# Performance work log

Measured on AMD Instinct MI355X. Metric: run time of the kernel, lower is better.

Reference implementation:

```python
import jax, jax.numpy as jnp
import numpy as np

N, IN_DIM, OUT_DIM, HEADS = 8192, 256, 256, 2
C = OUT_DIM // HEADS  # per-head channel dim (concat=True)
ALPHA = 0.2
NEG = -9e15


def setup_inputs() -> dict:
    key = jax.random.key(0)
    ks = jax.random.split(key, 9)
    h = jax.random.normal(ks[0], (N, IN_DIM), dtype=jnp.float32)
    adj = jax.random.randint(ks[1], (N, N), 0, 2, dtype=jnp.int32)
    # torch nn.Linear weights are [out, in]; xavier-like scale
    def xav(k, shape):
        fan_in, fan_out = shape[1], shape[0]
        s = 1.414 * np.sqrt(6.0 / (fan_in + fan_out))
        return jax.random.uniform(k, shape, jnp.float32, -s, s)
    W1 = xav(ks[2], (HEADS * C, IN_DIM))
    W2 = xav(ks[3], (HEADS * C, IN_DIM))
    W3 = xav(ks[4], (HEADS * C, IN_DIM))
    b1 = jnp.zeros((HEADS * C,), jnp.float32)
    b2 = jnp.zeros((HEADS * C,), jnp.float32)
    b3 = jnp.zeros((HEADS * C,), jnp.float32)
    sa = 1.414 * np.sqrt(6.0 / (HEADS + 2 * C))
    a = jax.random.uniform(ks[5], (HEADS, 2 * C), jnp.float32, -sa, sa)
    return {"h": h, "adj": adj, "W1": W1, "b1": b1, "W2": W2, "b2": b2,
            "W3": W3, "b3": b3, "a": a}


def reference(h, adj, W1, b1, W2, b2, W3, b3, a):
    n = h.shape[0]
    W1h = (h @ W1.T + b1).reshape(n, HEADS, C)  # [N,H,C]
    W2h = (h @ W2.T + b2).reshape(n, HEADS, C)
    W3h = (h @ W3.T + b3).reshape(n, HEADS, C)
    # eij = a . [W1h_i || W2h_j] decomposes into per-node scores
    a1, a2 = a[:, :C], a[:, C:]
    s1 = jnp.einsum('nhc,hc->nh', W1h, a1)  # [N,H]
    s2 = jnp.einsum('nhc,hc->nh', W2h, a2)  # [N,H]
    e = jax.nn.leaky_relu(s1[:, None, :] + s2[None, :, :], ALPHA)  # [N,N,H]
    e = jnp.where(adj[:, :, None] == 1, e, NEG)
    att = jax.nn.softmax(e, axis=1)  # softmax over source dim j (dim=1)
    # dropout is identity in eval mode (training=False)
    h_prime = jnp.einsum('ijh,jhc->ihc', att, W3h)  # [N,H,C]
    return h_prime.reshape(n, HEADS * C)
```

## Files before the change

kernel.cpp:

```cpp
#include <hip/hip_runtime.h>
#include <hip/hip_bf16.h>

#define NN 8192
#define LOG2E 1.44269504088896f
#define S_SPLIT 8
#define JC 1024
#define NT 32

typedef __attribute__((ext_vector_type(8))) short short8;
typedef __attribute__((ext_vector_type(4))) float f32x4;

static __device__ __forceinline__ float bf2f(unsigned short u) {
    union { unsigned int i; float f; } v; v.i = ((unsigned int)u) << 16; return v.f;
}
static __device__ __forceinline__ unsigned short f2bf(float f) {
    union { float f; unsigned int i; } v; v.f = f;
    unsigned int lsb = (v.i >> 16) & 1u;
    v.i += 0x7fffu + lsb;
    return (unsigned short)(v.i >> 16);
}
static __device__ __forceinline__ unsigned int cvtpk(float lo, float hi) {
    unsigned int r;
    asm("v_cvt_pk_bf16_f32 %0, %1, %2" : "=v"(r) : "v"(lo), "v"(hi));
    return r;
}
static __device__ __forceinline__ float fexp2(float x) { return __builtin_amdgcn_exp2f(x); }

static __device__ __forceinline__ void cvt8(const float* __restrict__ p, short8& hi, short8& lo) {
    float4 u = *(const float4*)p;
    float4 v = *(const float4*)(p + 4);
    float f[8] = {u.x, u.y, u.z, u.w, v.x, v.y, v.z, v.w};
#pragma unroll
    for (int j = 0; j < 8; ++j) {
        unsigned short hb = f2bf(f[j]);
        hi[j] = (short)hb;
        lo[j] = (short)f2bf(f[j] - bf2f(hb));
    }
}

__global__ __launch_bounds__(256) void pack_kernel(const int* __restrict__ adj,
                                                   unsigned int* __restrict__ abits,
                                                   const float* __restrict__ W3,
                                                   unsigned short* __restrict__ w3hi,
                                                   unsigned short* __restrict__ w3lo) {
    int b = blockIdx.x;
    if (b < 8192) {
        int w = b * 256 + threadIdx.x;
        const int* src = adj + (size_t)w * 32;
        unsigned int bits = 0;
#pragma unroll
        for (int k = 0; k < 8; ++k) {
            int4 v = *(const int4*)(src + k * 4);
            bits |= (unsigned int)(v.x & 1) << (k * 4 + 0);
            bits |= (unsigned int)(v.y & 1) << (k * 4 + 1);
            bits |= (unsigned int)(v.z & 1) << (k * 4 + 2);
            bits |= (unsigned int)(v.w & 1) << (k * 4 + 3);
        }
        abits[w] = bits;
    } else {
        int i = (b - 8192) * 256 + threadIdx.x;
        float f = W3[i];
        unsigned short hb = f2bf(f);
        w3hi[i] = hb;
        w3lo[i] = f2bf(f - bf2f(hb));
    }
}

__global__ void prep_partial(const float* __restrict__ W1, const float* __restrict__ W2,
                             const float* __restrict__ a,
                             float* __restrict__ v1p, float* __restrict__ v2p) {
    int b = blockIdx.x;
    int t = threadIdx.x;
    int hh = t >> 8, k = t & 255;
    int c0 = (b & 7) * 16;
    const float* W = (b < 8) ? W1 : W2;
    int aoff = (b < 8) ? 0 : 128;
    float acc = 0.f;
    for (int c = c0; c < c0 + 16; ++c)
        acc += W[(size_t)(hh * 128 + c) * 256 + k] * a[hh * 256 + aoff + c];
    ((b < 8) ? v1p : v2p)[(b & 7) * 512 + t] = acc;
}

__global__ void prep_reduce(const float* __restrict__ b1, const float* __restrict__ b2,
                            const float* __restrict__ a,
                            const float* __restrict__ v1p, const float* __restrict__ v2p,
                            float* __restrict__ v1, float* __restrict__ v2, float* __restrict__ bd) {
    int t = threadIdx.x;
    float a1 = 0.f, a2 = 0.f;
    for (int b = 0; b < 8; ++b) { a1 += v1p[b * 512 + t]; a2 += v2p[b * 512 + t]; }
    v1[t] = a1;
    v2[t] = a2;
    int g = t >> 7;
    int hh = g >> 1, which = g & 1, c = t & 127;
    float prod = which ? b2[hh * 128 + c] * a[hh * 256 + 128 + c]
                       : b1[hh * 128 + c] * a[hh * 256 + c];
#pragma unroll
    for (int off = 1; off < 64; off <<= 1) prod += __shfl_xor(prod, off);
    __shared__ float ws[8];
    if ((t & 63) == 0) ws[t >> 6] = prod;
    __syncthreads();
    if (t < 4) bd[t] = ws[2 * t] + ws[2 * t + 1];
}

__global__ __launch_bounds__(256) void s_kernel(const float* __restrict__ hmat,
                         const float* __restrict__ v1, const float* __restrict__ v2,
                         const float* __restrict__ bd,
                         float* __restrict__ s1o, float* __restrict__ s2o) {
    int w = threadIdx.x >> 6, l = threadIdx.x & 63;
    int n = blockIdx.x * 4 + w;
    float4 hv  = *(const float4*)(hmat + (size_t)n * 256 + l * 4);
    float4 va0 = *(const float4*)(v1 + l * 4);
    float4 va1 = *(const float4*)(v1 + 256 + l * 4);
    float4 vb0 = *(const float4*)(v2 + l * 4);
    float4 vb1 = *(const float4*)(v2 + 256 + l * 4);
    float s10 = hv.x*va0.x + hv.y*va0.y + hv.z*va0.z + hv.w*va0.w;
    float s11 = hv.x*va1.x + hv.y*va1.y + hv.z*va1.z + hv.w*va1.w;
    float s20 = hv.x*vb0.x + hv.y*vb0.y + hv.z*vb0.z + hv.w*vb0.w;
    float s21 = hv.x*vb1.x + hv.y*vb1.y + hv.z*vb1.z + hv.w*vb1.w;
#pragma unroll
    for (int off = 1; off < 64; off <<= 1) {
        s10 += __shfl_xor(s10, off);
        s11 += __shfl_xor(s11, off);
        s20 += __shfl_xor(s20, off);
        s21 += __shfl_xor(s21, off);
    }
    if (l == 0) {
        s1o[n*2 + 0] = (s10 + bd[0]) * LOG2E;
        s1o[n*2 + 1] = (s11 + bd[2]) * LOG2E;
        s2o[n]       = (s20 + bd[1]) * LOG2E;
        s2o[NN + n]  = (s21 + bd[3]) * LOG2E;
    }
}

__global__ __launch_bounds__(256) void w3_kernel(const float* __restrict__ hmat,
                                                 const unsigned short* __restrict__ w3hi,
                                                 const unsigned short* __restrict__ w3lo,
                                                 const float* __restrict__ b3,
                                                 unsigned short* __restrict__ w3b) {
    int tid = threadIdx.x;
    int w = tid >> 6, l = tid & 63;
    int m = l & 15, kq = l >> 4;
    int n0 = (blockIdx.x * 2 + (w & 1)) * 16;
    int c0 = (w >> 1) * 8;
    f32x4 acc[8];
#pragma unroll
    for (int ct = 0; ct < 8; ++ct) acc[ct] = (f32x4){0.f, 0.f, 0.f, 0.f};
    for (int k0 = 0; k0 < 256; k0 += 32) {
        short8 ahi, alo;
        cvt8(hmat + (size_t)(n0 + m) * 256 + k0 + kq * 8, ahi, alo);
#pragma unroll
        for (int ct = 0; ct < 8; ++ct) {
            int c = (c0 + ct) * 16 + m;
            short8 bhi = *(const short8*)&w3hi[(size_t)c * 256 + k0 + kq * 8];
            short8 blo = *(const short8*)&w3lo[(size_t)c * 256 + k0 + kq * 8];
            acc[ct] = __builtin_amdgcn_mfma_f32_16x16x32_bf16(ahi, bhi, acc[ct], 0, 0, 0);
            acc[ct] = __builtin_amdgcn_mfma_f32_16x16x32_bf16(alo, bhi, acc[ct], 0, 0, 0);
            acc[ct] = __builtin_amdgcn_mfma_f32_16x16x32_bf16(ahi, blo, acc[ct], 0, 0, 0);
        }
    }
#pragma unroll
    for (int ct = 0; ct < 8; ++ct) {
        int c = (c0 + ct) * 16 + m;
        float bias = b3[c];
#pragma unroll
        for (int e = 0; e < 4; ++e) {
            int n = n0 + kq * 4 + e;
            size_t idx = ((size_t)(n >> 5) * 16 + (c >> 4)) * 512 + (size_t)((((n >> 3) & 3) * 16 + m) * 8 + (n & 7));
            w3b[idx] = f2bf(acc[ct][e] + bias);
        }
    }
}

__global__ __launch_bounds__(256, 4) void attn_fused(
        const unsigned int* __restrict__ abits, const float* __restrict__ s1a,
        const float* __restrict__ s2h, const unsigned short* __restrict__ w3b,
        unsigned short* __restrict__ pacc, float* __restrict__ pden)
{
    __shared__ float s2t[2][JC];
    __shared__ unsigned int abt[64][33];

    const int tid = threadIdx.x;
    const int ln = tid & 63;
    const int m = ln & 15, kq = ln >> 4;
    const int cg = tid >> 6;
    const int hw = cg >> 1;
    const int sidx = blockIdx.x & 7;
    const int i0 = (blockIdx.x >> 3) * 64;
    const int j0 = sidx * JC;

    float s1r[4];
#pragma unroll
    for (int rt = 0; rt < 4; ++rt) s1r[rt] = s1a[(i0 + rt * 16 + m) * 2 + hw];

    const unsigned short* w3p = w3b + ((size_t)(j0 >> 5) * 16 + cg * 4) * 512 + ln * 8;

    f32x4 acc[4][4];
#pragma unroll
    for (int rt = 0; rt < 4; ++rt)
#pragma unroll
        for (int f = 0; f < 4; ++f) acc[rt][f] = (f32x4){0.f, 0.f, 0.f, 0.f};
    float den[4] = {0.f, 0.f, 0.f, 0.f};

    for (int x = tid; x < 2 * JC; x += 256) {
        int h = x >> 10, j = x & (JC - 1);
        s2t[h][j] = s2h[(size_t)h * NN + j0 + j];
    }
    for (int x = tid; x < 64 * 32; x += 256) {
        int rr = x >> 5, tt = x & 31;
        abt[rr][tt] = abits[(size_t)(i0 + rr) * 256 + (j0 >> 5) + tt];
    }
    __syncthreads();

    for (int t = 0; t < NT; ++t) {
        const unsigned short* bp = w3p + (size_t)t * 8192;
        short8 bf0 = *(const short8*)(bp);
        short8 bf1 = *(const short8*)(bp + 512);
        short8 bf2 = *(const short8*)(bp + 1024);
        short8 bf3 = *(const short8*)(bp + 1536);
        float4 sA = *(const float4*)&s2t[hw][t * 32 + kq * 8];
        float4 sB = *(const float4*)&s2t[hw][t * 32 + kq * 8 + 4];
        float sj[8] = {sA.x, sA.y, sA.z, sA.w, sB.x, sB.y, sB.z, sB.w};
#pragma unroll
        for (int rt = 0; rt < 4; ++rt) {
            unsigned int bits = abt[rt * 16 + m][t] >> (kq * 8);
            const float sr = s1r[rt];
            union { short8 v; unsigned int u[4]; } A;
            float dd = 0.f;
#pragma unroll
            for (int e = 0; e < 4; ++e) {
                float x0 = sr + sj[2 * e];     x0 = fmaxf(x0, 0.2f * x0);
                float x1 = sr + sj[2 * e + 1]; x1 = fmaxf(x1, 0.2f * x1);
                float p0 = (bits >> (2 * e))     & 1u ? fexp2(x0) : 0.f;
                float p1 = (bits >> (2 * e + 1)) & 1u ? fexp2(x1) : 0.f;
                A.u[e] = cvtpk(p0, p1);
                dd += p0 + p1;
            }
            den[rt] += dd;
            __builtin_amdgcn_s_setprio(1);
            acc[rt][0] = __builtin_amdgcn_mfma_f32_16x16x32_bf16(A.v, bf0, acc[rt][0], 0, 0, 0);
            acc[rt][1] = __builtin_amdgcn_mfma_f32_16x16x32_bf16(A.v, bf1, acc[rt][1], 0, 0, 0);
            acc[rt][2] = __builtin_amdgcn_mfma_f32_16x16x32_bf16(A.v, bf2, acc[rt][2], 0, 0, 0);
            acc[rt][3] = __builtin_amdgcn_mfma_f32_16x16x32_bf16(A.v, bf3, acc[rt][3], 0, 0, 0);
            __builtin_amdgcn_s_setprio(0);
        }
    }

#pragma unroll
    for (int rt = 0; rt < 4; ++rt) {
        den[rt] += __shfl_xor(den[rt], 16);
        den[rt] += __shfl_xor(den[rt], 32);
    }
    if ((cg & 1) == 0 && kq == 0) {
#pragma unroll
        for (int rt = 0; rt < 4; ++rt)
            pden[((size_t)sidx * NN + i0 + rt * 16 + m) * 2 + hw] = den[rt];
    }
    size_t pb_ = (size_t)sidx * NN * 256;
#pragma unroll
    for (int rt = 0; rt < 4; ++rt)
#pragma unroll
        for (int e = 0; e < 4; ++e) {
            int row = i0 + rt * 16 + kq * 4 + e;
#pragma unroll
            for (int f = 0; f < 4; ++f) {
                int col = cg * 64 + f * 16 + m;
                __builtin_nontemporal_store(f2bf(acc[rt][f][e]), &pacc[pb_ + (size_t)row * 256 + col]);
            }
        }
}

__global__ void combine_kernel(const unsigned short* __restrict__ pacc, const float* __restrict__ pden,
                               float* __restrict__ out) {
    size_t idx = ((size_t)blockIdx.x * 256 + threadIdx.x) * 8;
    int i = (int)(idx >> 8);
    int c = (int)(idx & 255);
    int hh = c >> 7;
    float acc[8];
#pragma unroll
    for (int e = 0; e < 8; ++e) acc[e] = 0.f;
    float den = 0.f;
    for (int s = 0; s < S_SPLIT; ++s) {
        uint4 v = *(const uint4*)&pacc[(size_t)s * NN * 256 + idx];
        unsigned int uu[4] = {v.x, v.y, v.z, v.w};
#pragma unroll
        for (int q = 0; q < 4; ++q) {
            acc[2*q]   += bf2f((unsigned short)(uu[q] & 0xffff));
            acc[2*q+1] += bf2f((unsigned short)(uu[q] >> 16));
        }
        den += pden[((size_t)s * NN + i) * 2 + hh];
    }
    float r = 1.f / den;
    float4 o0 = {acc[0]*r, acc[1]*r, acc[2]*r, acc[3]*r};
    float4 o1 = {acc[4]*r, acc[5]*r, acc[6]*r, acc[7]*r};
    *(float4*)&out[idx] = o0;
    *(float4*)&out[idx + 4] = o1;
}

extern "C" void kernel_launch(void* const* d_in, const int* in_sizes, int n_in,
                              void* d_out, int out_size, void* d_ws, size_t ws_size,
                              hipStream_t stream) {
    const float* hmat = (const float*)d_in[0];
    const int*   adj  = (const int*)d_in[1];
    const float* W1   = (const float*)d_in[2];
    const float* b1   = (const float*)d_in[3];
    const float* W2   = (const float*)d_in[4];
    const float* b2   = (const float*)d_in[5];
    const float* W3   = (const float*)d_in[6];
    const float* b3   = (const float*)d_in[7];
    const float* a    = (const float*)d_in[8];
    float* out = (float*)d_out;

    char* p = (char*)d_ws;
    float* v1   = (float*)p; p += 2048;
    float* v2   = (float*)p; p += 2048;
    float* bd   = (float*)p; p += 256;
    float* s1   = (float*)p; p += (size_t)NN * 2 * sizeof(float);
    float* s2h  = (float*)p; p += (size_t)NN * 2 * sizeof(float);
    float* v1p  = (float*)p; p += 8 * 512 * sizeof(float);
    float* v2p  = (float*)p; p += 8 * 512 * sizeof(float);
    unsigned short* w3hi = (unsigned short*)p; p += 65536 * 2;
    unsigned short* w3lo = (unsigned short*)p; p += 65536 * 2;
    unsigned short* w3b  = (unsigned short*)p; p += (size_t)NN * 256 * 2;
    unsigned int* abits  = (unsigned int*)p;   p += (size_t)NN * 256 * sizeof(unsigned int);
    float* pden = (float*)p; p += (size_t)S_SPLIT * NN * 2 * sizeof(float);
    unsigned short* pacc = (unsigned short*)p;

    pack_kernel<<<8192 + 256, 256, 0, stream>>>(adj, abits, W3, w3hi, w3lo);
    prep_partial<<<16, 512, 0, stream>>>(W1, W2, a, v1p, v2p);
    prep_reduce<<<1, 512, 0, stream>>>(b1, b2, a, v1p, v2p, v1, v2, bd);
    s_kernel<<<NN / 4, 256, 0, stream>>>(hmat, v1, v2, bd, s1, s2h);
    w3_kernel<<<256, 256, 0, stream>>>(hmat, w3hi, w3lo, b3, w3b);
    attn_fused<<<(NN / 64) * S_SPLIT, 256, 0, stream>>>(abits, s1, s2h, w3b, pacc, pden);
    combine_kernel<<<(NN * 256) / (256 * 8), 256, 0, stream>>>(pacc, pden, out);
}
```

Before: 188.5 us.

## Swap MFMA operand roles so each wave owns 16 rows and all channels

The attention kernel is restructured so each wave handles 16 query rows across all 256 channels. The exp/leaky-relu work for each (row, j) pair is now computed once per wave instead of being split across waves, with W3 as the A operand and probabilities as B. This leaves the output transposed, so partial results are stored channel-major and the combine kernel is rewritten to read that transposed layout and divide by per-row denominators held in shared memory. The intent is to cut redundant VALU exp and bit-extraction work, at the cost of 16 global W3 fragment loads per iteration, higher accumulator register pressure, and scattered 2-byte transposed stores.

```diff
diff --git a/kernel.cpp b/kernel.cpp
--- a/kernel.cpp
+++ b/kernel.cpp
@@ -174,7 +174,7 @@
 __global__ __launch_bounds__(256, 4) void attn_fused(
         const unsigned int* __restrict__ abits, const float* __restrict__ s1a,
         const float* __restrict__ s2h, const unsigned short* __restrict__ w3b,
-        unsigned short* __restrict__ pacc, float* __restrict__ pden)
+        unsigned short* __restrict__ paccT, float* __restrict__ pden)
 {
     __shared__ float s2t[2][JC];
     __shared__ unsigned int abt[64][33];
@@ -182,24 +182,20 @@
     const int tid = threadIdx.x;
     const int ln = tid & 63;
     const int m = ln & 15, kq = ln >> 4;
-    const int cg = tid >> 6;
-    const int hw = cg >> 1;
+    const int wv = tid >> 6;
     const int sidx = blockIdx.x & 7;
     const int i0 = (blockIdx.x >> 3) * 64;
     const int j0 = sidx * JC;
-
-    float s1r[4];
-#pragma unroll
-    for (int rt = 0; rt < 4; ++rt) s1r[rt] = s1a[(i0 + rt * 16 + m) * 2 + hw];
-
-    const unsigned short* w3p = w3b + ((size_t)(j0 >> 5) * 16 + cg * 4) * 512 + ln * 8;
-
-    f32x4 acc[4][4];
-#pragma unroll
-    for (int rt = 0; rt < 4; ++rt)
-#pragma unroll
-        for (int f = 0; f < 4; ++f) acc[rt][f] = (f32x4){0.f, 0.f, 0.f, 0.f};
-    float den[4] = {0.f, 0.f, 0.f, 0.f};
+    const int irow = i0 + wv * 16 + m;
+
+    const float s1r0 = s1a[irow * 2 + 0];
+    const float s1r1 = s1a[irow * 2 + 1];
+    const unsigned short* w3p = w3b + (size_t)(j0 >> 5) * 16 * 512 + ln * 8;
+
+    f32x4 acc[16];
+#pragma unroll
+    for (int ct = 0; ct < 16; ++ct) acc[ct] = (f32x4){0.f, 0.f, 0.f, 0.f};
+    float d0 = 0.f, d1 = 0.f;
 
     for (int x = tid; x < 2 * JC; x += 256) {
         int h = x >> 10, j = x & (JC - 1);
@@ -212,88 +208,87 @@
     __syncthreads();
 
     for (int t = 0; t < NT; ++t) {
+        unsigned int bits = abt[wv * 16 + m][t] >> (kq * 8);
+        float4 sv00 = *(const float4*)&s2t[0][t * 32 + kq * 8];
+        float4 sv01 = *(const float4*)&s2t[0][t * 32 + kq * 8 + 4];
+        float4 sv10 = *(const float4*)&s2t[1][t * 32 + kq * 8];
+        float4 sv11 = *(const float4*)&s2t[1][t * 32 + kq * 8 + 4];
+        float f0[8] = {sv00.x, sv00.y, sv00.z, sv00.w, sv01.x, sv01.y, sv01.z, sv01.w};
+        float f1[8] = {sv10.x, sv10.y, sv10.z, sv10.w, sv11.x, sv11.y, sv11.z, sv11.w};
+        union { short8 v; unsigned int u[4]; } PA, PB;
+        float dd0 = 0.f, dd1 = 0.f;
+#pragma unroll
+        for (int q = 0; q < 4; ++q) {
+            float x0 = s1r0 + f0[2*q];     x0 = fmaxf(x0, 0.2f * x0);
+            float x1 = s1r0 + f0[2*q+1];   x1 = fmaxf(x1, 0.2f * x1);
+            float p0 = (bits >> (2*q))     & 1u ? fexp2(x0) : 0.f;
+            float p1 = (bits >> (2*q+1))   & 1u ? fexp2(x1) : 0.f;
+            PA.u[q] = cvtpk(p0, p1); dd0 += p0 + p1;
+            x0 = s1r1 + f1[2*q];     x0 = fmaxf(x0, 0.2f * x0);
+            x1 = s1r1 + f1[2*q+1];   x1 = fmaxf(x1, 0.2f * x1);
+            p0 = (bits >> (2*q))     & 1u ? fexp2(x0) : 0.f;
+            p1 = (bits >> (2*q+1))   & 1u ? fexp2(x1) : 0.f;
+            PB.u[q] = cvtpk(p0, p1); dd1 += p0 + p1;
+        }
+        d0 += dd0; d1 += dd1;
         const unsigned short* bp = w3p + (size_t)t * 8192;
-        short8 bf0 = *(const short8*)(bp);
-        short8 bf1 = *(const short8*)(bp + 512);
-        short8 bf2 = *(const short8*)(bp + 1024);
-        short8 bf3 = *(const short8*)(bp + 1536);
-        float4 sA = *(const float4*)&s2t[hw][t * 32 + kq * 8];
-        float4 sB = *(const float4*)&s2t[hw][t * 32 + kq * 8 + 4];
-        float sj[8] = {sA.x, sA.y, sA.z, sA.w, sB.x, sB.y, sB.z, sB.w};
-#pragma unroll
-        for (int rt = 0; rt < 4; ++rt) {
-            unsigned int bits = abt[rt * 16 + m][t] >> (kq * 8);
-            const float sr = s1r[rt];
-            union { short8 v; unsigned int u[4]; } A;
-            float dd = 0.f;
-#pragma unroll
-            for (int e = 0; e < 4; ++e) {
-                float x0 = sr + sj[2 * e];     x0 = fmaxf(x0, 0.2f * x0);
-                float x1 = sr + sj[2 * e + 1]; x1 = fmaxf(x1, 0.2f * x1);
-                float p0 = (bits >> (2 * e))     & 1u ? fexp2(x0) : 0.f;
-                float p1 = (bits >> (2 * e + 1)) & 1u ? fexp2(x1) : 0.f;
-                A.u[e] = cvtpk(p0, p1);
-                dd += p0 + p1;
+#pragma unroll
+        for (int ct = 0; ct < 16; ++ct) {
+            short8 aw = *(const short8*)(bp + ct * 512);
+            acc[ct] = __builtin_amdgcn_mfma_f32_16x16x32_bf16(aw, ct < 8 ? PA.v : PB.v, acc[ct], 0, 0, 0);
+        }
+    }
+
+    d0 += __shfl_xor(d0, 16); d0 += __shfl_xor(d0, 32);
+    d1 += __shfl_xor(d1, 16); d1 += __shfl_xor(d1, 32);
+    if (kq == 0) {
+        size_t base = ((size_t)sidx * NN + irow) * 2;
+        pden[base + 0] = d0;
+        pden[base + 1] = d1;
+    }
+    size_t pb_ = (size_t)sidx * NN * 256;
+#pragma unroll
+    for (int ct = 0; ct < 16; ++ct)
+#pragma unroll
+        for (int e = 0; e < 4; ++e) {
+            int c = ct * 16 + kq * 4 + e;
+            __builtin_nontemporal_store(f2bf(acc[ct][e]), &paccT[pb_ + (size_t)c * NN + irow]);
+        }
+}
+
+__global__ __launch_bounds__(256) void combine_kernel(const unsigned short* __restrict__ paccT,
+                                                      const float* __restrict__ pden,
+                                                      float* __restrict__ out) {
+    __shared__ float dsum[32][2];
+    int i0 = blockIdx.x * 32;
+    int c = threadIdx.x;
+    if (threadIdx.x < 64) {
+        int i = threadIdx.x >> 1, h = threadIdx.x & 1;
+        float d = 0.f;
+        for (int s = 0; s < S_SPLIT; ++s) d += pden[((size_t)s * NN + i0 + i) * 2 + h];
+        dsum[i][h] = d;
+    }
+    __syncthreads();
+    float acc[32];
+#pragma unroll
+    for (int e = 0; e < 32; ++e) acc[e] = 0.f;
+    for (int s = 0; s < S_SPLIT; ++s) {
+        const unsigned short* src = paccT + (size_t)s * NN * 256 + (size_t)c * NN + i0;
+#pragma unroll
+        for (int q = 0; q < 4; ++q) {
+            uint4 v = *(const uint4*)(src + q * 8);
+            unsigned int uu[4] = {v.x, v.y, v.z, v.w};
+#pragma unroll
+            for (int w = 0; w < 4; ++w) {
+                acc[q*8 + 2*w]     += bf2f((unsigned short)(uu[w] & 0xffff));
+                acc[q*8 + 2*w + 1] += bf2f((unsigned short)(uu[w] >> 16));
             }
-            den[rt] += dd;
-            __builtin_amdgcn_s_setprio(1);
-            acc[rt][0] = __builtin_amdgcn_mfma_f32_16x16x32_bf16(A.v, bf0, acc[rt][0], 0, 0, 0);
-            acc[rt][1] = __builtin_amdgcn_mfma_f32_16x16x32_bf16(A.v, bf1, acc[rt][1], 0, 0, 0);
-            acc[rt][2] = __builtin_amdgcn_mfma_f32_16x16x32_bf16(A.v, bf2, acc[rt][2], 0, 0, 0);
-            acc[rt][3] = __builtin_amdgcn_mfma_f32_16x16x32_bf16(A.v, bf3, acc[rt][3], 0, 0, 0);
-            __builtin_amdgcn_s_setprio(0);
-        }
-    }
-
-#pragma unroll
-    for (int rt = 0; rt < 4; ++rt) {
-        den[rt] += __shfl_xor(den[rt], 16);
-        den[rt] += __shfl_xor(den[rt], 32);
-    }
-    if ((cg & 1) == 0 && kq == 0) {
-#pragma unroll
-        for (int rt = 0; rt < 4; ++rt)
-            pden[((size_t)sidx * NN + i0 + rt * 16 + m) * 2 + hw] = den[rt];
-    }
-    size_t pb_ = (size_t)sidx * NN * 256;
-#pragma unroll
-    for (int rt = 0; rt < 4; ++rt)
-#pragma unroll
-        for (int e = 0; e < 4; ++e) {
-            int row = i0 + rt * 16 + kq * 4 + e;
-#pragma unroll
-            for (int f = 0; f < 4; ++f) {
-                int col = cg * 64 + f * 16 + m;
-                __builtin_nontemporal_store(f2bf(acc[rt][f][e]), &pacc[pb_ + (size_t)row * 256 + col]);
-            }
-        }
-}
-
-__global__ void combine_kernel(const unsigned short* __restrict__ pacc, const float* __restrict__ pden,
-                               float* __restrict__ out) {
-    size_t idx = ((size_t)blockIdx.x * 256 + threadIdx.x) * 8;
-    int i = (int)(idx >> 8);
-    int c = (int)(idx & 255);
+        }
+    }
     int hh = c >> 7;
-    float acc[8];
-#pragma unroll
-    for (int e = 0; e < 8; ++e) acc[e] = 0.f;
-    float den = 0.f;
-    for (int s = 0; s < S_SPLIT; ++s) {
-        uint4 v = *(const uint4*)&pacc[(size_t)s * NN * 256 + idx];
-        unsigned int uu[4] = {v.x, v.y, v.z, v.w};
-#pragma unroll
-        for (int q = 0; q < 4; ++q) {
-            acc[2*q]   += bf2f((unsigned short)(uu[q] & 0xffff));
-            acc[2*q+1] += bf2f((unsigned short)(uu[q] >> 16));
-        }
-        den += pden[((size_t)s * NN + i) * 2 + hh];
-    }
-    float r = 1.f / den;
-    float4 o0 = {acc[0]*r, acc[1]*r, acc[2]*r, acc[3]*r};
-    float4 o1 = {acc[4]*r, acc[5]*r, acc[6]*r, acc[7]*r};
-    *(float4*)&out[idx] = o0;
-    *(float4*)&out[idx + 4] = o1;
+#pragma unroll
+    for (int i = 0; i < 32; ++i)
+        out[(size_t)(i0 + i) * 256 + c] = acc[i] / dsum[i][hh];
 }
 
 extern "C" void kernel_launch(void* const* d_in, const int* in_sizes, int n_in,
@@ -323,13 +318,13 @@
     unsigned short* w3b  = (unsigned short*)p; p += (size_t)NN * 256 * 2;
     unsigned int* abits  = (unsigned int*)p;   p += (size_t)NN * 256 * sizeof(unsigned int);
     float* pden = (float*)p; p += (size_t)S_SPLIT * NN * 2 * sizeof(float);
-    unsigned short* pacc = (unsigned short*)p;
+    unsigned short* paccT = (unsigned short*)p;
 
     pack_kernel<<<8192 + 256, 256, 0, stream>>>(adj, abits, W3, w3hi, w3lo);
     prep_partial<<<16, 512, 0, stream>>>(W1, W2, a, v1p, v2p);
     prep_reduce<<<1, 512, 0, stream>>>(b1, b2, a, v1p, v2p, v1, v2, bd);
     s_kernel<<<NN / 4, 256, 0, stream>>>(hmat, v1, v2, bd, s1, s2h);
     w3_kernel<<<256, 256, 0, stream>>>(hmat, w3hi, w3lo, b3, w3b);
-    attn_fused<<<(NN / 64) * S_SPLIT, 256, 0, stream>>>(abits, s1, s2h, w3b, pacc, pden);
-    combine_kernel<<<(NN * 256) / (256 * 8), 256, 0, stream>>>(pacc, pden, out);
-}
+    attn_fused<<<(NN / 64) * S_SPLIT, 256, 0, stream>>>(abits, s1, s2h, w3b, paccT, pden);
+    combine_kernel<<<NN / 32, 256, 0, stream>>>(paccT, pden, out);
+}
```

Result: slower. 193.8 us (+2.8%).

## Remap attention waves to row-halves per head to remove duplicated exp work

Applied to the files above, without the earlier changes.

Each wave now owns 32 rows and a full head's 128 output channels, instead of 64 rows and a 64-channel quarter. Each attention probability is therefore computed once per block rather than twice. The cost is twice as many W3 fragment loads per wave per step. The launch grid also becomes 2D, with the j-split on the y axis, which changes block scheduling order.

```diff
diff --git a/kernel.cpp b/kernel.cpp
--- a/kernel.cpp
+++ b/kernel.cpp
@@ -182,24 +182,23 @@
     const int tid = threadIdx.x;
     const int ln = tid & 63;
     const int m = ln & 15, kq = ln >> 4;
-    const int cg = tid >> 6;
-    const int hw = cg >> 1;
-    const int sidx = blockIdx.x & 7;
-    const int i0 = (blockIdx.x >> 3) * 64;
+    const int wv = tid >> 6;
+    const int rg = wv & 1, hd = wv >> 1;
+    const int i0 = blockIdx.x * 64;
+    const int sidx = blockIdx.y;
     const int j0 = sidx * JC;
-
-    float s1r[4];
-#pragma unroll
-    for (int rt = 0; rt < 4; ++rt) s1r[rt] = s1a[(i0 + rt * 16 + m) * 2 + hw];
-
-    const unsigned short* w3p = w3b + ((size_t)(j0 >> 5) * 16 + cg * 4) * 512 + ln * 8;
-
-    f32x4 acc[4][4];
-#pragma unroll
-    for (int rt = 0; rt < 4; ++rt)
-#pragma unroll
-        for (int f = 0; f < 4; ++f) acc[rt][f] = (f32x4){0.f, 0.f, 0.f, 0.f};
-    float den[4] = {0.f, 0.f, 0.f, 0.f};
+    const int rowA = rg * 32 + m, rowB = rg * 32 + 16 + m;
+
+    const float s1r0 = s1a[(i0 + rowA) * 2 + hd];
+    const float s1r1 = s1a[(i0 + rowB) * 2 + hd];
+    const unsigned short* w3p = w3b + ((size_t)(j0 >> 5) * 16 + hd * 8) * 512 + ln * 8;
+
+    f32x4 acc[2][8];
+#pragma unroll
+    for (int rt = 0; rt < 2; ++rt)
+#pragma unroll
+        for (int f = 0; f < 8; ++f) acc[rt][f] = (f32x4){0.f, 0.f, 0.f, 0.f};
+    float dd0 = 0.f, dd1 = 0.f;
 
     for (int x = tid; x < 2 * JC; x += 256) {
         int h = x >> 10, j = x & (JC - 1);
@@ -212,58 +211,49 @@
     __syncthreads();
 
     for (int t = 0; t < NT; ++t) {
+        unsigned int bits0 = abt[rowA][t] >> (kq * 8);
+        unsigned int bits1 = abt[rowB][t] >> (kq * 8);
+        float4 svA = *(const float4*)&s2t[hd][t * 32 + kq * 8];
+        float4 svB = *(const float4*)&s2t[hd][t * 32 + kq * 8 + 4];
+        float sj[8] = {svA.x, svA.y, svA.z, svA.w, svB.x, svB.y, svB.z, svB.w};
+        union { short8 v; unsigned int u[4]; } PA, PB;
+#pragma unroll
+        for (int q = 0; q < 4; ++q) {
+            float x0 = s1r0 + sj[2*q];     x0 = fmaxf(x0, 0.2f * x0);
+            float x1 = s1r0 + sj[2*q+1];   x1 = fmaxf(x1, 0.2f * x1);
+            float p0 = (bits0 >> (2*q))   & 1u ? fexp2(x0) : 0.f;
+            float p1 = (bits0 >> (2*q+1)) & 1u ? fexp2(x1) : 0.f;
+            PA.u[q] = cvtpk(p0, p1); dd0 += p0 + p1;
+            x0 = s1r1 + sj[2*q];     x0 = fmaxf(x0, 0.2f * x0);
+            x1 = s1r1 + sj[2*q+1];   x1 = fmaxf(x1, 0.2f * x1);
+            p0 = (bits1 >> (2*q))   & 1u ? fexp2(x0) : 0.f;
+            p1 = (bits1 >> (2*q+1)) & 1u ? fexp2(x1) : 0.f;
+            PB.u[q] = cvtpk(p0, p1); dd1 += p0 + p1;
+        }
         const unsigned short* bp = w3p + (size_t)t * 8192;
-        short8 bf0 = *(const short8*)(bp);
-        short8 bf1 = *(const short8*)(bp + 512);
-        short8 bf2 = *(const short8*)(bp + 1024);
-        short8 bf3 = *(const short8*)(bp + 1536);
-        float4 sA = *(const float4*)&s2t[hw][t * 32 + kq * 8];
-        float4 sB = *(const float4*)&s2t[hw][t * 32 + kq * 8 + 4];
-        float sj[8] = {sA.x, sA.y, sA.z, sA.w, sB.x, sB.y, sB.z, sB.w};
-#pragma unroll
-        for (int rt = 0; rt < 4; ++rt) {
-            unsigned int bits = abt[rt * 16 + m][t] >> (kq * 8);
-            const float sr = s1r[rt];
-            union { short8 v; unsigned int u[4]; } A;
-            float dd = 0.f;
-#pragma unroll
-            for (int e = 0; e < 4; ++e) {
-                float x0 = sr + sj[2 * e];     x0 = fmaxf(x0, 0.2f * x0);
-                float x1 = sr + sj[2 * e + 1]; x1 = fmaxf(x1, 0.2f * x1);
-                float p0 = (bits >> (2 * e))     & 1u ? fexp2(x0) : 0.f;
-                float p1 = (bits >> (2 * e + 1)) & 1u ? fexp2(x1) : 0.f;
-                A.u[e] = cvtpk(p0, p1);
-                dd += p0 + p1;
-            }
-            den[rt] += dd;
-            __builtin_amdgcn_s_setprio(1);
-            acc[rt][0] = __builtin_amdgcn_mfma_f32_16x16x32_bf16(A.v, bf0, acc[rt][0], 0, 0, 0);
-            acc[rt][1] = __builtin_amdgcn_mfma_f32_16x16x32_bf16(A.v, bf1, acc[rt][1], 0, 0, 0);
-            acc[rt][2] = __builtin_amdgcn_mfma_f32_16x16x32_bf16(A.v, bf2, acc[rt][2], 0, 0, 0);
-            acc[rt][3] = __builtin_amdgcn_mfma_f32_16x16x32_bf16(A.v, bf3, acc[rt][3], 0, 0, 0);
-            __builtin_amdgcn_s_setprio(0);
-        }
-    }
-
-#pragma unroll
-    for (int rt = 0; rt < 4; ++rt) {
-        den[rt] += __shfl_xor(den[rt], 16);
-        den[rt] += __shfl_xor(den[rt], 32);
-    }
-    if ((cg & 1) == 0 && kq == 0) {
-#pragma unroll
-        for (int rt = 0; rt < 4; ++rt)
-            pden[((size_t)sidx * NN + i0 + rt * 16 + m) * 2 + hw] = den[rt];
+#pragma unroll
+        for (int f = 0; f < 8; ++f) {
+            short8 bf = *(const short8*)(bp + f * 512);
+            acc[0][f] = __builtin_amdgcn_mfma_f32_16x16x32_bf16(PA.v, bf, acc[0][f], 0, 0, 0);
+            acc[1][f] = __builtin_amdgcn_mfma_f32_16x16x32_bf16(PB.v, bf, acc[1][f], 0, 0, 0);
+        }
+    }
+
+    dd0 += __shfl_xor(dd0, 16); dd0 += __shfl_xor(dd0, 32);
+    dd1 += __shfl_xor(dd1, 16); dd1 += __shfl_xor(dd1, 32);
+    if (kq == 0) {
+        pden[((size_t)sidx * NN + i0 + rowA) * 2 + hd] = dd0;
+        pden[((size_t)sidx * NN + i0 + rowB) * 2 + hd] = dd1;
     }
     size_t pb_ = (size_t)sidx * NN * 256;
 #pragma unroll
-    for (int rt = 0; rt < 4; ++rt)
+    for (int rt = 0; rt < 2; ++rt)
 #pragma unroll
         for (int e = 0; e < 4; ++e) {
-            int row = i0 + rt * 16 + kq * 4 + e;
-#pragma unroll
-            for (int f = 0; f < 4; ++f) {
-                int col = cg * 64 + f * 16 + m;
+            int row = i0 + rg * 32 + rt * 16 + kq * 4 + e;
+#pragma unroll
+            for (int f = 0; f < 8; ++f) {
+                int col = hd * 128 + f * 16 + m;
                 __builtin_nontemporal_store(f2bf(acc[rt][f][e]), &pacc[pb_ + (size_t)row * 256 + col]);
             }
         }
@@ -330,6 +320,6 @@
     prep_reduce<<<1, 512, 0, stream>>>(b1, b2, a, v1p, v2p, v1, v2, bd);
     s_kernel<<<NN / 4, 256, 0, stream>>>(hmat, v1, v2, bd, s1, s2h);
     w3_kernel<<<256, 256, 0, stream>>>(hmat, w3hi, w3lo, b3, w3b);
-    attn_fused<<<(NN / 64) * S_SPLIT, 256, 0, stream>>>(abits, s1, s2h, w3b, pacc, pden);
+    attn_fused<<<dim3(NN / 64, S_SPLIT), 256, 0, stream>>>(abits, s1, s2h, w3b, pacc, pden);
     combine_kernel<<<(NN * 256) / (256 * 8), 256, 0, stream>>>(pacc, pden, out);
 }
```

New measurement: 160.9 us. 1.17x faster.
